# Kernel tuning notes

Hardware: AMD Instinct MI355X
Metric: run time of the kernel (lower is better)

Reference implementation:

```python
import jax, jax.numpy as jnp
import numpy as np


def setup_inputs() -> dict:
    key = jax.random.key(0)
    k1, k2, k3 = jax.random.split(key, 3)
    B, T, H = 64, 512, 1024
    return {
        "encoder_out": jax.random.normal(k1, (B, T, H), dtype=jnp.float32),
        "W_ih": jax.random.normal(k2, (3 * H, H), dtype=jnp.float32) * (1.0 / np.sqrt(H)),
        "W_hh": jax.random.normal(k3, (3 * H, H), dtype=jnp.float32) * (1.0 / np.sqrt(H)),
        "b_ih": jnp.zeros((3 * H,), dtype=jnp.float32),
        "b_hh": jnp.zeros((3 * H,), dtype=jnp.float32),
    }


def reference(encoder_out, W_ih, W_hh, b_ih, b_hh):
    # PyTorch GRUCell semantics; gate order in stacked weights is (r, z, n).
    B, T, H = encoder_out.shape

    # Batch the input-to-hidden projection across all timesteps: [B,T,3H]
    x_proj = jnp.einsum("bth,gh->btg", encoder_out, W_ih) + b_ih
    x_proj_t = jnp.swapaxes(x_proj, 0, 1)  # [T, B, 3H] for scan

    W_hh_T = W_hh.T  # [H, 3H]

    def step(h, xp):
        # recurrent projection: [B, 3H]
        h_proj = h @ W_hh_T + b_hh
        xr, xz, xn = jnp.split(xp, 3, axis=-1)
        hr, hz, hn = jnp.split(h_proj, 3, axis=-1)
        r = jax.nn.sigmoid(xr + hr)
        z = jax.nn.sigmoid(xz + hz)
        n = jnp.tanh(xn + r * hn)
        h_new = (1.0 - z) * n + z * h
        return h_new, h_new

    h0 = jnp.zeros((B, H), dtype=encoder_out.dtype)
    _, h_seq = jax.lax.scan(step, h0, x_proj_t)  # [T, B, H]
    return jnp.swapaxes(h_seq, 0, 1)  # [B, T, H]
```

## Files before the change

kernel.cpp:

```cpp
#include <hip/hip_runtime.h>
#include <hip/hip_bf16.h>


typedef short bf16x8 __attribute__((ext_vector_type(8)));
typedef float f32x4 __attribute__((ext_vector_type(4)));

#define NB 64
#define NT 512
#define NH 1024
#define NG 3072

static __device__ __forceinline__ float bf2f(unsigned short u) {
    unsigned int x = ((unsigned int)u) << 16;
    float f;
    __builtin_memcpy(&f, &x, sizeof(f));
    return f;
}
static __device__ __forceinline__ unsigned short f2bf(float f) {
    unsigned int x;
    __builtin_memcpy(&x, &f, sizeof(x));
    x += 0x7fffu + ((x >> 16) & 1u);
    return (unsigned short)(x >> 16);
}

static __device__ __forceinline__ f32x4 mfma16(bf16x8 a, bf16x8 b, f32x4 c) {
    return __builtin_amdgcn_mfma_f32_16x16x32_bf16(a, b, c, 0, 0, 0);
}

#define GLD16(gp, lp) __builtin_amdgcn_global_load_lds( \
    (const __attribute__((address_space(1))) void*)(gp), \
    (__attribute__((address_space(3))) void*)(lp), 16, 0, 0)

__global__ void k_fill_sentinel(float* __restrict__ o, long n) {
    long i = (long)blockIdx.x * blockDim.x + threadIdx.x;
    if (i < n) o[i] = 12345.0f;
}

__global__ void k_convert(const float* __restrict__ in, unsigned short* __restrict__ o, int n) {
    int i = blockIdx.x * blockDim.x + threadIdx.x;
    if (i < n) o[i] = f2bf(in[i]);
}

__global__ void k_convert_enc(const float* __restrict__ enc, unsigned short* __restrict__ o) {
    long i = (long)blockIdx.x * blockDim.x + threadIdx.x;
    if (i >= (long)NB * NT * NH) return;
    int h = (int)(i % NH);
    long bt = i / NH;
    int t = (int)(bt % NT);
    int b = (int)(bt / NT);
    o[((long)t * NB + b) * NH + h] = f2bf(enc[i]);
}

#define SYNC_WORDS (4 * NB * NH / 2 + 128)
__global__ void k_init_sync(unsigned int* __restrict__ base) {
    int i = blockIdx.x * blockDim.x + threadIdx.x;
    if (i < SYNC_WORDS) base[i] = 0u;
}

__global__ __launch_bounds__(256) void k_xproj(
    const unsigned short* __restrict__ X,
    const unsigned short* __restrict__ W,
    const float* __restrict__ bias,
    unsigned short* __restrict__ xp)
{
    __shared__ unsigned short As[128 * 32];
    __shared__ unsigned short Bs[128 * 32];

    const int tid  = threadIdx.x;
    const int lane = tid & 63;
    const int wv   = tid >> 6;
    const int l16  = lane & 15;
    const int lq   = lane >> 4;
    const int wr   = wv >> 1;
    const int wc   = wv & 1;
    const int n0   = blockIdx.x * 128;
    const int m0   = blockIdx.y * 128;

    f32x4 acc[4][4];
#pragma unroll
    for (int mi = 0; mi < 4; ++mi)
#pragma unroll
        for (int nj = 0; nj < 4; ++nj) acc[mi][nj] = (f32x4){0.f, 0.f, 0.f, 0.f};

    const int r0 = tid >> 2;
    const int c0e = (tid & 3) * 8;
    const int r1 = (256 + tid) >> 2;

    for (int k0 = 0; k0 < NH; k0 += 32) {
        GLD16(X + (size_t)(m0 + r0) * NH + k0 + c0e, &As[tid * 8]);
        GLD16(X + (size_t)(m0 + r1) * NH + k0 + c0e, &As[(256 + tid) * 8]);
        GLD16(W + (size_t)(n0 + r0) * NH + k0 + c0e, &Bs[tid * 8]);
        GLD16(W + (size_t)(n0 + r1) * NH + k0 + c0e, &Bs[(256 + tid) * 8]);
        __syncthreads();

        bf16x8 a[4], b[4];
#pragma unroll
        for (int mi = 0; mi < 4; ++mi)
            a[mi] = *(const bf16x8*)&As[(wr * 64 + mi * 16 + l16) * 32 + lq * 8];
#pragma unroll
        for (int nj = 0; nj < 4; ++nj)
            b[nj] = *(const bf16x8*)&Bs[(wc * 64 + nj * 16 + l16) * 32 + lq * 8];
#pragma unroll
        for (int mi = 0; mi < 4; ++mi)
#pragma unroll
            for (int nj = 0; nj < 4; ++nj)
                acc[mi][nj] = mfma16(a[mi], b[nj], acc[mi][nj]);
        __syncthreads();
    }

#pragma unroll
    for (int nj = 0; nj < 4; ++nj) {
        int n = n0 + wc * 64 + nj * 16 + l16;
        float bv = bias[n];
        int g   = n >> 10;
        int u   = n & 1023;
        int ugb = u >> 5;
        int ui  = u & 31;
#pragma unroll
        for (int mi = 0; mi < 4; ++mi) {
#pragma unroll
            for (int i = 0; i < 4; ++i) {
                int m = m0 + wr * 64 + mi * 16 + lq * 4 + i;
                int t = m >> 6;
                int b = m & 63;
                xp[(((long)t * 32 + ugb) * 64 + b) * 96 + g * 32 + ui] = f2bf(acc[mi][nj][i] + bv);
            }
        }
    }
}

__global__ __launch_bounds__(512, 1) void k_scan(
    const unsigned short* __restrict__ Whh,
    const float* __restrict__ bhh,
    const unsigned short* __restrict__ xp,
    unsigned short* __restrict__ hring,
    unsigned* __restrict__ flags,
    float* __restrict__ out)
{
    const int tid  = threadIdx.x;
    const int lane = tid & 63;
    const int wv   = tid >> 6;
    const int l16  = lane & 15;
    const int lq   = lane >> 4;
    const int bid  = blockIdx.x;
    const int mg   = bid >> 5;
    const int ug   = bid & 31;
    const int m0   = mg * 16;
    const int u0   = ug * 32;
    const int kc0  = wv * 128;

    bf16x8 Bf[3][2][4];
#pragma unroll
    for (int g = 0; g < 3; ++g)
#pragma unroll
        for (int f = 0; f < 2; ++f)
#pragma unroll
            for (int ks = 0; ks < 4; ++ks)
                Bf[g][f][ks] = *(const bf16x8*)(Whh + (long)(g * NH + u0 + f * 16 + l16) * NH + kc0 + ks * 32 + lq * 8);
#pragma unroll
    for (int g = 0; g < 3; ++g)
#pragma unroll
        for (int f = 0; f < 2; ++f)
#pragma unroll
            for (int ks = 0; ks < 4; ++ks)
                asm volatile("" : "+v"(Bf[g][f][ks]));

    const int u_loc = tid & 31;
    const int b_loc = tid >> 5;
    const int b_own = m0 + b_loc;
    const int u_own = u0 + u_loc;
    float bh[3];
#pragma unroll
    for (int g = 0; g < 3; ++g) bh[g] = bhh[g * NH + u_own];
    float hf = 0.0f;

    const int lane_t = (b_loc >> 2) * 16 + (u_loc & 15);
    const int i_t    = b_loc & 3;
    const int shalf  = (u_loc >> 4) * 3;

    const unsigned* fp_my = flags + mg * 32 + wv * 4 + (lane & 3);

    __shared__ f32x4 red[8][6][64];

    for (int t = 0; t < NT; ++t) {
        const int slot_r = (t + 3) & 3;
        const int slot_w = t & 3;

        const unsigned short* xpp = xp + (((long)t * 32 + ug) * 64 + b_own) * 96;
        float xr = bf2f(xpp[u_loc]);
        float xz = bf2f(xpp[32 + u_loc]);
        float xn = bf2f(xpp[64 + u_loc]);

        if (t > 0) {
            for (;;) {
                unsigned fv;
                asm volatile("global_load_dword %0, %1, off sc0 sc1\n\ts_waitcnt vmcnt(0)"
                             : "=v"(fv) : "v"(fp_my) : "memory");
                if (__all(fv >= (unsigned)t)) break;
            }
        }

        const unsigned short* hp = hring + ((slot_r * NB + m0 + l16) * NH + kc0 + lq * 8);
        bf16x8 av[4];
        asm volatile(
            "global_load_dwordx4 %0, %4, off sc0 sc1\n\t"
            "global_load_dwordx4 %1, %4, off offset:64 sc0 sc1\n\t"
            "global_load_dwordx4 %2, %4, off offset:128 sc0 sc1\n\t"
            "global_load_dwordx4 %3, %4, off offset:192 sc0 sc1\n\t"
            "s_waitcnt vmcnt(0)"
            : "=&v"(av[0]), "=&v"(av[1]), "=&v"(av[2]), "=&v"(av[3])
            : "v"(hp) : "memory");

        f32x4 acc[2][3];
#pragma unroll
        for (int f = 0; f < 2; ++f)
#pragma unroll
            for (int g = 0; g < 3; ++g) acc[f][g] = (f32x4){0.f, 0.f, 0.f, 0.f};
#pragma unroll
        for (int ks = 0; ks < 4; ++ks)
#pragma unroll
            for (int f = 0; f < 2; ++f)
#pragma unroll
                for (int g = 0; g < 3; ++g)
                    acc[f][g] = mfma16(av[ks], Bf[g][f][ks], acc[f][g]);

#pragma unroll
        for (int f = 0; f < 2; ++f)
#pragma unroll
            for (int g = 0; g < 3; ++g) red[wv][f * 3 + g][lane] = acc[f][g];
        __syncthreads();

        float pre[3];
#pragma unroll
        for (int g = 0; g < 3; ++g) {
            float s = 0.0f;
#pragma unroll
            for (int w = 0; w < 8; ++w) s += red[w][shalf + g][lane_t][i_t];
            pre[g] = s + bh[g];
        }

        float r = 1.0f / (1.0f + __expf(-(xr + pre[0])));
        float z = 1.0f / (1.0f + __expf(-(xz + pre[1])));
        float narg = xn + r * pre[2];
        float nval = 1.0f - 2.0f / (__expf(2.0f * narg) + 1.0f);
        float hnew = (1.0f - z) * nval + z * hf;
        hf = hnew;

        {
            unsigned short* hw = hring + (slot_w * NB + b_own) * NH + u_own;
            unsigned hv = (unsigned)f2bf(hnew);
            asm volatile("global_store_short %0, %1, off sc0 sc1"
                         :: "v"(hw), "v"(hv) : "memory");
        }
        asm volatile("s_waitcnt vmcnt(0)" ::: "memory");
        __syncthreads();
        if (tid == 0) {
            unsigned fv = (unsigned)(t + 1);
            asm volatile("global_store_dword %0, %1, off sc0 sc1"
                         :: "v"(flags + mg * 32 + ug), "v"(fv) : "memory");
        }
        out[((long)b_own * NT + t) * NH + u_own] = hnew;
    }
}

extern "C" void kernel_launch(void* const* d_in, const int* in_sizes, int n_in,
                              void* d_out, int out_size, void* d_ws, size_t ws_size,
                              hipStream_t stream) {
    const float* enc = (const float*)d_in[0];
    const float* Wih = (const float*)d_in[1];
    const float* Whh = (const float*)d_in[2];
    const float* bih = (const float*)d_in[3];
    const float* bhh = (const float*)d_in[4];
    float* out = (float*)d_out;

    char* p = (char*)d_ws;
    unsigned short* enc_t = (unsigned short*)p; p += (size_t)NT * NB * NH * 2;
    unsigned short* xp    = (unsigned short*)p; p += (size_t)NT * NB * NG * 2;
    unsigned short* wih_b = (unsigned short*)p; p += (size_t)NG * NH * 2;
    unsigned short* whh_b = (unsigned short*)p; p += (size_t)NG * NH * 2;
    size_t need = (size_t)(p - (char*)d_ws);

    unsigned short* hring = enc_t;
    unsigned* flags = (unsigned*)(hring + (size_t)4 * NB * NH);

    if (ws_size < need) {
        long n = (long)out_size;
        k_fill_sentinel<<<(int)((n + 255) / 256), 256, 0, stream>>>(out, n);
        return;
    }

    {
        int n = NG * NH;
        k_convert<<<(n + 255) / 256, 256, 0, stream>>>(Wih, wih_b, n);
        k_convert<<<(n + 255) / 256, 256, 0, stream>>>(Whh, whh_b, n);
        long ne = (long)NB * NT * NH;
        k_convert_enc<<<(int)((ne + 255) / 256), 256, 0, stream>>>(enc, enc_t);
    }

    {
        dim3 grid(NG / 128, (NT * NB) / 128);
        k_xproj<<<grid, 256, 0, stream>>>(enc_t, wih_b, bih, xp);
    }

    k_init_sync<<<(SYNC_WORDS + 255) / 256, 256, 0, stream>>>((unsigned*)hring);

    k_scan<<<128, 512, 0, stream>>>(whh_b, bhh, xp, hring, flags, out);
}
```

Measured before the change: 2.290 ms.

## Fuse input projection into recurrent scan kernel, removing separate GEMM pass

Removes the separate encoder transpose/convert kernel and the batched x-projection GEMM, and instead computes each timestep's input projection inside the persistent scan kernel before waiting on the recurrence flag. The x-projection partials go into the same LDS reduction as the recurrent ones, with the n-gate input and hidden parts kept separate. This avoids writing and re-reading the large projected-input buffer and several launches. In exchange, each step now loads W_ih fragments from global or cache and fp32 encoder rows, and converts them to bf16, on a latency-bound serial path. Only 128 blocks are available to do that GEMM work.

```diff
diff --git a/kernel.cpp b/kernel.cpp
--- a/kernel.cpp
+++ b/kernel.cpp
@@ -27,10 +27,6 @@
     return __builtin_amdgcn_mfma_f32_16x16x32_bf16(a, b, c, 0, 0, 0);
 }
 
-#define GLD16(gp, lp) __builtin_amdgcn_global_load_lds( \
-    (const __attribute__((address_space(1))) void*)(gp), \
-    (__attribute__((address_space(3))) void*)(lp), 16, 0, 0)
-
 __global__ void k_fill_sentinel(float* __restrict__ o, long n) {
     long i = (long)blockIdx.x * blockDim.x + threadIdx.x;
     if (i < n) o[i] = 12345.0f;
@@ -39,16 +35,6 @@
 __global__ void k_convert(const float* __restrict__ in, unsigned short* __restrict__ o, int n) {
     int i = blockIdx.x * blockDim.x + threadIdx.x;
     if (i < n) o[i] = f2bf(in[i]);
-}
-
-__global__ void k_convert_enc(const float* __restrict__ enc, unsigned short* __restrict__ o) {
-    long i = (long)blockIdx.x * blockDim.x + threadIdx.x;
-    if (i >= (long)NB * NT * NH) return;
-    int h = (int)(i % NH);
-    long bt = i / NH;
-    int t = (int)(bt % NT);
-    int b = (int)(bt / NT);
-    o[((long)t * NB + b) * NH + h] = f2bf(enc[i]);
 }
 
 #define SYNC_WORDS (4 * NB * NH / 2 + 128)
@@ -57,82 +43,12 @@
     if (i < SYNC_WORDS) base[i] = 0u;
 }
 
-__global__ __launch_bounds__(256) void k_xproj(
-    const unsigned short* __restrict__ X,
-    const unsigned short* __restrict__ W,
-    const float* __restrict__ bias,
-    unsigned short* __restrict__ xp)
-{
-    __shared__ unsigned short As[128 * 32];
-    __shared__ unsigned short Bs[128 * 32];
-
-    const int tid  = threadIdx.x;
-    const int lane = tid & 63;
-    const int wv   = tid >> 6;
-    const int l16  = lane & 15;
-    const int lq   = lane >> 4;
-    const int wr   = wv >> 1;
-    const int wc   = wv & 1;
-    const int n0   = blockIdx.x * 128;
-    const int m0   = blockIdx.y * 128;
-
-    f32x4 acc[4][4];
-#pragma unroll
-    for (int mi = 0; mi < 4; ++mi)
-#pragma unroll
-        for (int nj = 0; nj < 4; ++nj) acc[mi][nj] = (f32x4){0.f, 0.f, 0.f, 0.f};
-
-    const int r0 = tid >> 2;
-    const int c0e = (tid & 3) * 8;
-    const int r1 = (256 + tid) >> 2;
-
-    for (int k0 = 0; k0 < NH; k0 += 32) {
-        GLD16(X + (size_t)(m0 + r0) * NH + k0 + c0e, &As[tid * 8]);
-        GLD16(X + (size_t)(m0 + r1) * NH + k0 + c0e, &As[(256 + tid) * 8]);
-        GLD16(W + (size_t)(n0 + r0) * NH + k0 + c0e, &Bs[tid * 8]);
-        GLD16(W + (size_t)(n0 + r1) * NH + k0 + c0e, &Bs[(256 + tid) * 8]);
-        __syncthreads();
-
-        bf16x8 a[4], b[4];
-#pragma unroll
-        for (int mi = 0; mi < 4; ++mi)
-            a[mi] = *(const bf16x8*)&As[(wr * 64 + mi * 16 + l16) * 32 + lq * 8];
-#pragma unroll
-        for (int nj = 0; nj < 4; ++nj)
-            b[nj] = *(const bf16x8*)&Bs[(wc * 64 + nj * 16 + l16) * 32 + lq * 8];
-#pragma unroll
-        for (int mi = 0; mi < 4; ++mi)
-#pragma unroll
-            for (int nj = 0; nj < 4; ++nj)
-                acc[mi][nj] = mfma16(a[mi], b[nj], acc[mi][nj]);
-        __syncthreads();
-    }
-
-#pragma unroll
-    for (int nj = 0; nj < 4; ++nj) {
-        int n = n0 + wc * 64 + nj * 16 + l16;
-        float bv = bias[n];
-        int g   = n >> 10;
-        int u   = n & 1023;
-        int ugb = u >> 5;
-        int ui  = u & 31;
-#pragma unroll
-        for (int mi = 0; mi < 4; ++mi) {
-#pragma unroll
-            for (int i = 0; i < 4; ++i) {
-                int m = m0 + wr * 64 + mi * 16 + lq * 4 + i;
-                int t = m >> 6;
-                int b = m & 63;
-                xp[(((long)t * 32 + ugb) * 64 + b) * 96 + g * 32 + ui] = f2bf(acc[mi][nj][i] + bv);
-            }
-        }
-    }
-}
-
 __global__ __launch_bounds__(512, 1) void k_scan(
+    const unsigned short* __restrict__ Wih,
     const unsigned short* __restrict__ Whh,
+    const float* __restrict__ bih,
     const float* __restrict__ bhh,
-    const unsigned short* __restrict__ xp,
+    const float* __restrict__ enc,
     unsigned short* __restrict__ hring,
     unsigned* __restrict__ flags,
     float* __restrict__ out)
@@ -169,27 +85,51 @@
     const int b_loc = tid >> 5;
     const int b_own = m0 + b_loc;
     const int u_own = u0 + u_loc;
-    float bh[3];
-#pragma unroll
-    for (int g = 0; g < 3; ++g) bh[g] = bhh[g * NH + u_own];
+    float bi[3], bh[3];
+#pragma unroll
+    for (int g = 0; g < 3; ++g) { bi[g] = bih[g * NH + u_own]; bh[g] = bhh[g * NH + u_own]; }
     float hf = 0.0f;
 
     const int lane_t = (b_loc >> 2) * 16 + (u_loc & 15);
     const int i_t    = b_loc & 3;
-    const int shalf  = (u_loc >> 4) * 3;
+    const int shalf  = (u_loc >> 4) * 4;
 
     const unsigned* fp_my = flags + mg * 32 + wv * 4 + (lane & 3);
 
-    __shared__ f32x4 red[8][6][64];
+    const float* enc_base = enc + ((size_t)(m0 + l16) * NT) * NH + kc0 + lq * 8;
+    const unsigned short* wih_base = Wih + (size_t)(u0 + l16) * NH + kc0 + lq * 8;
+
+    __shared__ f32x4 red[8][8][64];
 
     for (int t = 0; t < NT; ++t) {
         const int slot_r = (t + 3) & 3;
         const int slot_w = t & 3;
 
-        const unsigned short* xpp = xp + (((long)t * 32 + ug) * 64 + b_own) * 96;
-        float xr = bf2f(xpp[u_loc]);
-        float xz = bf2f(xpp[32 + u_loc]);
-        float xn = bf2f(xpp[64 + u_loc]);
+        f32x4 accx[2][3];
+#pragma unroll
+        for (int f = 0; f < 2; ++f)
+#pragma unroll
+            for (int g = 0; g < 3; ++g) accx[f][g] = (f32x4){0.f, 0.f, 0.f, 0.f};
+
+        const float* ep = enc_base + (size_t)t * NH;
+#pragma unroll
+        for (int ks = 0; ks < 4; ++ks) {
+            float4 fa = *(const float4*)(ep + ks * 32);
+            float4 fb = *(const float4*)(ep + ks * 32 + 4);
+            union { unsigned short s[8]; bf16x8 v; } cv;
+            cv.s[0] = f2bf(fa.x); cv.s[1] = f2bf(fa.y);
+            cv.s[2] = f2bf(fa.z); cv.s[3] = f2bf(fa.w);
+            cv.s[4] = f2bf(fb.x); cv.s[5] = f2bf(fb.y);
+            cv.s[6] = f2bf(fb.z); cv.s[7] = f2bf(fb.w);
+            bf16x8 avx = cv.v;
+#pragma unroll
+            for (int g = 0; g < 3; ++g)
+#pragma unroll
+                for (int f = 0; f < 2; ++f) {
+                    bf16x8 bx = *(const bf16x8*)(wih_base + ((size_t)g * NH + f * 16) * NH + ks * 32);
+                    accx[f][g] = mfma16(avx, bx, accx[f][g]);
+                }
+        }
 
         if (t > 0) {
             for (;;) {
@@ -211,37 +151,40 @@
             : "=&v"(av[0]), "=&v"(av[1]), "=&v"(av[2]), "=&v"(av[3])
             : "v"(hp) : "memory");
 
-        f32x4 acc[2][3];
-#pragma unroll
-        for (int f = 0; f < 2; ++f)
-#pragma unroll
-            for (int g = 0; g < 3; ++g) acc[f][g] = (f32x4){0.f, 0.f, 0.f, 0.f};
+        f32x4 acch[2][3];
+#pragma unroll
+        for (int f = 0; f < 2; ++f)
+#pragma unroll
+            for (int g = 0; g < 3; ++g) acch[f][g] = (f32x4){0.f, 0.f, 0.f, 0.f};
 #pragma unroll
         for (int ks = 0; ks < 4; ++ks)
 #pragma unroll
             for (int f = 0; f < 2; ++f)
 #pragma unroll
                 for (int g = 0; g < 3; ++g)
-                    acc[f][g] = mfma16(av[ks], Bf[g][f][ks], acc[f][g]);
-
-#pragma unroll
-        for (int f = 0; f < 2; ++f)
-#pragma unroll
-            for (int g = 0; g < 3; ++g) red[wv][f * 3 + g][lane] = acc[f][g];
+                    acch[f][g] = mfma16(av[ks], Bf[g][f][ks], acch[f][g]);
+
+#pragma unroll
+        for (int f = 0; f < 2; ++f) {
+            red[wv][f * 4 + 0][lane] = acch[f][0] + accx[f][0];
+            red[wv][f * 4 + 1][lane] = acch[f][1] + accx[f][1];
+            red[wv][f * 4 + 2][lane] = acch[f][2];
+            red[wv][f * 4 + 3][lane] = accx[f][2];
+        }
         __syncthreads();
 
-        float pre[3];
-#pragma unroll
-        for (int g = 0; g < 3; ++g) {
-            float s = 0.0f;
-#pragma unroll
-            for (int w = 0; w < 8; ++w) s += red[w][shalf + g][lane_t][i_t];
-            pre[g] = s + bh[g];
-        }
-
-        float r = 1.0f / (1.0f + __expf(-(xr + pre[0])));
-        float z = 1.0f / (1.0f + __expf(-(xz + pre[1])));
-        float narg = xn + r * pre[2];
+        float s_r = 0.f, s_z = 0.f, s_hn = 0.f, s_xn = 0.f;
+#pragma unroll
+        for (int w = 0; w < 8; ++w) {
+            s_r  += red[w][shalf + 0][lane_t][i_t];
+            s_z  += red[w][shalf + 1][lane_t][i_t];
+            s_hn += red[w][shalf + 2][lane_t][i_t];
+            s_xn += red[w][shalf + 3][lane_t][i_t];
+        }
+
+        float r = 1.0f / (1.0f + __expf(-(s_r + bi[0] + bh[0])));
+        float z = 1.0f / (1.0f + __expf(-(s_z + bi[1] + bh[1])));
+        float narg = (s_xn + bi[2]) + r * (s_hn + bh[2]);
         float nval = 1.0f - 2.0f / (__expf(2.0f * narg) + 1.0f);
         float hnew = (1.0f - z) * nval + z * hf;
         hf = hnew;
@@ -274,14 +217,11 @@
     float* out = (float*)d_out;
 
     char* p = (char*)d_ws;
-    unsigned short* enc_t = (unsigned short*)p; p += (size_t)NT * NB * NH * 2;
-    unsigned short* xp    = (unsigned short*)p; p += (size_t)NT * NB * NG * 2;
     unsigned short* wih_b = (unsigned short*)p; p += (size_t)NG * NH * 2;
     unsigned short* whh_b = (unsigned short*)p; p += (size_t)NG * NH * 2;
+    unsigned short* hring = (unsigned short*)p; p += (size_t)4 * NB * NH * 2;
+    unsigned* flags = (unsigned*)p; p += 128 * 4;
     size_t need = (size_t)(p - (char*)d_ws);
-
-    unsigned short* hring = enc_t;
-    unsigned* flags = (unsigned*)(hring + (size_t)4 * NB * NH);
 
     if (ws_size < need) {
         long n = (long)out_size;
@@ -293,16 +233,9 @@
         int n = NG * NH;
         k_convert<<<(n + 255) / 256, 256, 0, stream>>>(Wih, wih_b, n);
         k_convert<<<(n + 255) / 256, 256, 0, stream>>>(Whh, whh_b, n);
-        long ne = (long)NB * NT * NH;
-        k_convert_enc<<<(int)((ne + 255) / 256), 256, 0, stream>>>(enc, enc_t);
+        k_init_sync<<<(SYNC_WORDS + 255) / 256, 256, 0, stream>>>((unsigned*)hring);
     }
 
-    {
-        dim3 grid(NG / 128, (NT * NB) / 128);
-        k_xproj<<<grid, 256, 0, stream>>>(enc_t, wih_b, bih, xp);
-    }
-
-    k_init_sync<<<(SYNC_WORDS + 255) / 256, 256, 0, stream>>>((unsigned*)hring);
-
-    k_scan<<<128, 512, 0, stream>>>(whh_b, bhh, xp, hring, flags, out);
-}
+    k_scan<<<128, 512, 0, stream>>>(wih_b, whh_b, bih, bhh, enc,
+                                    hring, flags, out);
+}
```

Measured after the change: 3.548 ms. 1.55x slower.

## Use per-wave sync flags in scan, fuse prep kernels, swizzle xproj grid

Applied to the files above, without the earlier changes.

The three conversion kernels become one prep kernel, cutting launch count. The xproj GEMM now runs on a 1D grid with an XCD-aware swizzle to improve L2 reuse across chiplets. In the recurrent scan, each wave publishes its own completion flag right after its stores drain, and the block barrier moves to the end of the step. This takes the block-wide barrier off the critical path between finishing h and signalling peers, at the cost of more flag words to poll and a larger sync region.

```diff
diff --git a/kernel.cpp b/kernel.cpp
--- a/kernel.cpp
+++ b/kernel.cpp
@@ -36,22 +36,24 @@
     if (i < n) o[i] = 12345.0f;
 }
 
-__global__ void k_convert(const float* __restrict__ in, unsigned short* __restrict__ o, int n) {
-    int i = blockIdx.x * blockDim.x + threadIdx.x;
-    if (i < n) o[i] = f2bf(in[i]);
-}
-
-__global__ void k_convert_enc(const float* __restrict__ enc, unsigned short* __restrict__ o) {
+__global__ void k_prep(const float* __restrict__ enc, unsigned short* __restrict__ enc_t,
+                       const float* __restrict__ Wih, unsigned short* __restrict__ wih_b,
+                       const float* __restrict__ Whh, unsigned short* __restrict__ whh_b) {
     long i = (long)blockIdx.x * blockDim.x + threadIdx.x;
-    if (i >= (long)NB * NT * NH) return;
-    int h = (int)(i % NH);
-    long bt = i / NH;
-    int t = (int)(bt % NT);
-    int b = (int)(bt / NT);
-    o[((long)t * NB + b) * NH + h] = f2bf(enc[i]);
-}
-
-#define SYNC_WORDS (4 * NB * NH / 2 + 128)
+    if (i < (long)NB * NT * NH) {
+        int h = (int)(i % NH);
+        long bt = i / NH;
+        int t = (int)(bt % NT);
+        int b = (int)(bt / NT);
+        enc_t[((long)t * NB + b) * NH + h] = f2bf(enc[i]);
+    }
+    if (i < (long)NG * NH) {
+        wih_b[i] = f2bf(Wih[i]);
+        whh_b[i] = f2bf(Whh[i]);
+    }
+}
+
+#define SYNC_WORDS (4 * NB * NH / 2 + 1024)
 __global__ void k_init_sync(unsigned int* __restrict__ base) {
     int i = blockIdx.x * blockDim.x + threadIdx.x;
     if (i < SYNC_WORDS) base[i] = 0u;
@@ -73,8 +75,10 @@
     const int lq   = lane >> 4;
     const int wr   = wv >> 1;
     const int wc   = wv & 1;
-    const int n0   = blockIdx.x * 128;
-    const int m0   = blockIdx.y * 128;
+    const int bid  = blockIdx.x;
+    const int swz  = (bid & 7) * 768 + (bid >> 3);
+    const int n0   = (swz % 24) * 128;
+    const int m0   = (swz / 24) * 128;
 
     f32x4 acc[4][4];
 #pragma unroll
@@ -178,7 +182,8 @@
     const int i_t    = b_loc & 3;
     const int shalf  = (u_loc >> 4) * 3;
 
-    const unsigned* fp_my = flags + mg * 32 + wv * 4 + (lane & 3);
+    const unsigned* fp_my = flags + mg * 256 + (wv * 4 + ((lane & 31) >> 3)) * 8 + (lane & 7);
+    unsigned* fp_own = flags + mg * 256 + ug * 8 + wv;
 
     __shared__ f32x4 red[8][6][64];
 
@@ -253,13 +258,13 @@
                          :: "v"(hw), "v"(hv) : "memory");
         }
         asm volatile("s_waitcnt vmcnt(0)" ::: "memory");
-        __syncthreads();
-        if (tid == 0) {
+        if (lane == 0) {
             unsigned fv = (unsigned)(t + 1);
             asm volatile("global_store_dword %0, %1, off sc0 sc1"
-                         :: "v"(flags + mg * 32 + ug), "v"(fv) : "memory");
+                         :: "v"(fp_own), "v"(fv) : "memory");
         }
         out[((long)b_own * NT + t) * NH + u_own] = hnew;
+        __syncthreads();
     }
 }
 
@@ -290,17 +295,11 @@
     }
 
     {
-        int n = NG * NH;
-        k_convert<<<(n + 255) / 256, 256, 0, stream>>>(Wih, wih_b, n);
-        k_convert<<<(n + 255) / 256, 256, 0, stream>>>(Whh, whh_b, n);
         long ne = (long)NB * NT * NH;
-        k_convert_enc<<<(int)((ne + 255) / 256), 256, 0, stream>>>(enc, enc_t);
-    }
-
-    {
-        dim3 grid(NG / 128, (NT * NB) / 128);
-        k_xproj<<<grid, 256, 0, stream>>>(enc_t, wih_b, bih, xp);
-    }
+        k_prep<<<(int)((ne + 255) / 256), 256, 0, stream>>>(enc, enc_t, Wih, wih_b, Whh, whh_b);
+    }
+
+    k_xproj<<<6144, 256, 0, stream>>>(enc_t, wih_b, bih, xp);
 
     k_init_sync<<<(SYNC_WORDS + 255) / 256, 256, 0, stream>>>((unsigned*)hring);
 
```

New measurement: 2.613 ms. 1.14x slower.
